# Kernel optimization log

Hardware: AMD Instinct MI355X
Metric: run time of the kernel (lower is better)

## Reference

```python
import jax, jax.numpy as jnp
import numpy as np

# ---- dims (match init_kwargs / mamba_ssm Mamba2 defaults) ----
VOCAB = 32000
D_MODEL = 256
N_LAYERS = 2
D_STATE = 64   # N
D_CONV = 4
EXPAND = 2
MAX_SEQ = 1024
HEADDIM = 64   # P (Mamba2 default)
D_INNER = EXPAND * D_MODEL            # 512
NHEADS = D_INNER // HEADDIM           # 8
CONV_DIM = D_INNER + 2 * D_STATE      # 640 (ngroups=1)
D_IN_PROJ = 2 * D_INNER + 2 * D_STATE + NHEADS  # 1160
B, L = 2, 1024
EPS = 1e-5


def setup_inputs() -> dict:
    key = jax.random.key(0)
    ks = jax.random.split(key, 16)
    s = 0.02
    input_ids = jax.random.randint(ks[0], (B, L), 0, VOCAB)
    attention_mask = jnp.ones((B, L), jnp.float32)
    tok_emb = jax.random.normal(ks[1], (VOCAB, D_MODEL)) * s
    tok_emb = tok_emb.at[0].set(0.0)  # padding_idx=0
    pos_emb = jax.random.normal(ks[2], (MAX_SEQ, D_MODEL)) * s
    # per-direction (2) x per-layer (N_LAYERS) stacked Mamba2 params
    shp = (2, N_LAYERS)
    in_proj_w = jax.random.normal(ks[3], shp + (D_IN_PROJ, D_MODEL)) * s
    conv_w = jax.random.normal(ks[4], shp + (CONV_DIM, D_CONV)) * 0.1
    conv_b = jnp.zeros(shp + (CONV_DIM,))
    dt = jax.random.uniform(ks[5], shp + (NHEADS,), minval=1e-3, maxval=1e-1)
    dt_bias = dt + jnp.log(-jnp.expm1(-dt))  # inverse softplus
    A_log = jnp.log(jax.random.uniform(ks[6], shp + (NHEADS,), minval=1.0, maxval=16.0))
    D_param = jnp.ones(shp + (NHEADS,))
    norm_w = jnp.ones(shp + (D_INNER,))
    out_proj_w = jax.random.normal(ks[7], shp + (D_MODEL, D_INNER)) * s
    fusion_w = jax.random.normal(ks[8], (2 * D_MODEL, 2 * D_MODEL)) * s
    fusion_b = jnp.zeros((2 * D_MODEL,))
    ln_w = jnp.ones((D_MODEL,))
    ln_b = jnp.zeros((D_MODEL,))
    return dict(input_ids=input_ids, attention_mask=attention_mask,
                tok_emb=tok_emb, pos_emb=pos_emb, in_proj_w=in_proj_w,
                conv_w=conv_w, conv_b=conv_b, dt_bias=dt_bias, A_log=A_log,
                D_param=D_param, norm_w=norm_w, out_proj_w=out_proj_w,
                fusion_w=fusion_w, fusion_b=fusion_b, ln_w=ln_w, ln_b=ln_b)


def _mamba2_layer(u, in_w, cw, cb, dtb, A_log, Dp, nw, ow):
    """One Mamba2 block forward; u: (B,L,D_MODEL)."""
    bsz, seqlen, _ = u.shape
    zxbcdt = u @ in_w.T                                   # (B,L,1160)
    z = zxbcdt[..., :D_INNER]
    xBC = zxbcdt[..., D_INNER:D_INNER + CONV_DIM]
    dt = jax.nn.softplus(zxbcdt[..., D_INNER + CONV_DIM:] + dtb)  # (B,L,H)
    # causal depthwise conv over time + SiLU
    xc = jax.lax.conv_general_dilated(
        xBC.transpose(0, 2, 1), cw[:, None, :], (1,), [(D_CONV - 1, 0)],
        feature_group_count=CONV_DIM, dimension_numbers=('NCH', 'OIH', 'NCH'))
    xBC = jax.nn.silu(xc.transpose(0, 2, 1) + cb)
    x = xBC[..., :D_INNER].reshape(bsz, seqlen, NHEADS, HEADDIM)  # (B,L,H,P)
    Bm = xBC[..., D_INNER:D_INNER + D_STATE]                      # (B,L,N)
    Cm = xBC[..., D_INNER + D_STATE:]                             # (B,L,N)
    A = -jnp.exp(A_log)                                           # (H,)

    def step(h, inp):
        x_t, B_t, C_t, dt_t = inp          # (B,H,P),(B,N),(B,N),(B,H)
        dA = jnp.exp(dt_t * A)             # (B,H)
        h = h * dA[:, :, None, None] \
            + (dt_t[:, :, None] * x_t)[..., None] * B_t[:, None, None, :]
        y_t = jnp.einsum('bhpn,bn->bhp', h, C_t)
        return h, y_t

    h0 = jnp.zeros((bsz, NHEADS, HEADDIM, D_STATE), u.dtype)
    xs = (x.transpose(1, 0, 2, 3), Bm.transpose(1, 0, 2),
          Cm.transpose(1, 0, 2), dt.transpose(1, 0, 2))
    _, ys = jax.lax.scan(step, h0, xs)                 # (L,B,H,P)
    y = ys.transpose(1, 0, 2, 3) + Dp[None, None, :, None] * x
    y = y.reshape(bsz, seqlen, D_INNER)
    # gated RMSNorm (norm_before_gate=False)
    y = y * jax.nn.silu(z)
    y = y * jax.lax.rsqrt(jnp.mean(y * y, -1, keepdims=True) + EPS) * nw
    return y @ ow.T


def _stack(h, params, d):
    (in_w, cw, cb, dtb, alog, Dp, nw, ow) = params
    for i in range(N_LAYERS):
        h = _mamba2_layer(h, in_w[d, i], cw[d, i], cb[d, i], dtb[d, i],
                          alog[d, i], Dp[d, i], nw[d, i], ow[d, i])
    return h


def reference(input_ids, attention_mask, tok_emb, pos_emb, in_proj_w, conv_w,
              conv_b, dt_bias, A_log, D_param, norm_w, out_proj_w,
              fusion_w, fusion_b, ln_w, ln_b):
    bsz, seqlen = input_ids.shape
    h = tok_emb[input_ids] + pos_emb[:seqlen][None]        # (B,L,D)
    h = h * attention_mask[..., None]                      # dropout = identity (eval)
    params = (in_proj_w, conv_w, conv_b, dt_bias, A_log, D_param, norm_w, out_proj_w)
    fwd = _stack(h, params, 0)
    bwd = jnp.flip(_stack(jnp.flip(h, 1), params, 1), 1)
    combined = jnp.concatenate([fwd, bwd], -1)             # (B,L,2D)
    gate = jax.nn.sigmoid(combined @ fusion_w.T + fusion_b)
    gf, gb = gate[..., :D_MODEL], gate[..., D_MODEL:]
    fused = gf * fwd + gb * bwd
    mu = jnp.mean(fused, -1, keepdims=True)
    var = jnp.mean((fused - mu) ** 2, -1, keepdims=True)
    return (fused - mu) * jax.lax.rsqrt(var + EPS) * ln_w + ln_b
```

## Files before the change

kernel.cpp:

```cpp
#include <hip/hip_runtime.h>
#include <cstddef>

#define LSEQ    1024
#define DMODEL  256
#define DINNER  512
#define DSTATE  64
#define NHEADS  8
#define HEADDIM 64
#define CONVDIM 640
#define DINPROJ 1160
#define ROWS    2048
#define EPSF    1e-5f
#define NC      32
#define LC      32
#define XBCW    648
#define HROW    131072

#define WIN  593920
#define WOUT 262144
#define WF   262144
#define PSI  296960
#define PSO  131072

typedef _Float16 f16;
typedef f16   v8h __attribute__((ext_vector_type(8)));
typedef f16   v4h __attribute__((ext_vector_type(4)));
typedef float v4f __attribute__((ext_vector_type(4)));
#define MFMA16(a, b, c) __builtin_amdgcn_mfma_f32_16x16x32_f16(a, b, c, 0, 0, 0)

__device__ __forceinline__ float sigmoidf_(float x) { return 1.0f / (1.0f + expf(-x)); }
__device__ __forceinline__ float siluf_(float x)    { return x / (1.0f + expf(-x)); }
__device__ __forceinline__ float softplusf_(float x) {
    return x > 0.0f ? x + log1pf(expf(-x)) : log1pf(expf(x));
}
__device__ __forceinline__ void split16(float v, f16& h, f16& l) {
    h = (f16)v;
    l = (f16)((v - (float)h) * 4096.0f);
}

__global__ __launch_bounds__(256) void embed_kernel(
    const int* __restrict__ ids, const float* __restrict__ mask,
    const float* __restrict__ tok, const float* __restrict__ pos,
    f16* __restrict__ uh, f16* __restrict__ ul) {
    int row = blockIdx.x;
    int d = threadIdx.x;
    int b = row >> 10, t = row & 1023;
    int id = ids[row];
    float v = tok[(size_t)id * DMODEL + d] + pos[(size_t)t * DMODEL + d];
    v *= mask[row];
    f16 h, l; split16(v, h, l);
    size_t fwd = (size_t)row * DMODEL + d;
    size_t bwd = (size_t)ROWS * DMODEL + ((size_t)(b << 10) + (1023 - t)) * DMODEL + d;
    uh[fwd] = h; ul[fwd] = l;
    uh[bwd] = h; ul[bwd] = l;
}

__global__ __launch_bounds__(256) void wconv_kernel(
    const float* __restrict__ inw, const float* __restrict__ ow, const float* __restrict__ fw,
    f16* __restrict__ wb, int layer, int total) {
    int idx = (blockIdx.x * 256 + threadIdx.x) * 4;
#pragma unroll
    for (int e = idx; e < idx + 4; ++e) {
        if (e >= total) break;
        float v; f16 *dh, *dl; int off;
        if (e < WIN) {
            int d = e / PSI, r = e - d * PSI;
            v = inw[(size_t)(d * 2 + layer) * PSI + r];
            dh = wb; dl = wb + WIN; off = e;
        } else if (e < WIN + WOUT) {
            int e2 = e - WIN;
            int d = e2 / PSO, r = e2 - d * PSO;
            v = ow[(size_t)(d * 2 + layer) * PSO + r];
            dh = wb + 2 * WIN; dl = dh + WOUT; off = e2;
        } else {
            int e3 = e - WIN - WOUT;
            v = fw[e3];
            dh = wb + 2 * WIN + 2 * WOUT; dl = dh + WF; off = e3;
        }
        f16 h, l; split16(v, h, l);
        dh[off] = h; dl[off] = l;
    }
}

__global__ __launch_bounds__(256) void gemm_f16x3(
    const f16* __restrict__ Ah, const f16* __restrict__ Al, long sA,
    const f16* __restrict__ Wh, const f16* __restrict__ Wl, long sW,
    int N, int K, int Nsplit,
    float* __restrict__ O0, int ld0, long sO0,
    float* __restrict__ O1, int ld1, long sO1,
    f16* __restrict__ Ph, f16* __restrict__ Pl, int ldP, long sP,
    int has32, int haspair, int flipcomb) {
    int dir = blockIdx.z;
    Ah += (size_t)dir * sA; Al += (size_t)dir * sA;
    Wh += (size_t)dir * sW; Wl += (size_t)dir * sW;
    if (has32)  { O0 += (size_t)dir * sO0; O1 += (size_t)dir * sO1; }
    if (haspair){ Ph += (size_t)dir * sP;  Pl += (size_t)dir * sP; }

    __shared__ f16 sm[4 * 64 * 72];
    f16* As_h = sm;
    f16* As_l = sm + 64 * 72;
    f16* Ws_h = sm + 2 * 64 * 72;
    f16* Ws_l = sm + 3 * 64 * 72;

    int tid = threadIdx.x;
    int m0 = blockIdx.x * 64, n0 = blockIdx.y * 64;
    int srow = tid >> 2, sseg = tid & 3;
    int lane = tid & 63, w = tid >> 6;
    int wrow = (w >> 1) * 32, wcol = (w & 1) * 32;
    int q = lane >> 4, r16 = lane & 15;
    bool wok = (n0 + srow) < N;

    v4f accM[2][2], accX[2][2];
#pragma unroll
    for (int i = 0; i < 2; ++i)
#pragma unroll
        for (int j = 0; j < 2; ++j) { accM[i][j] = (v4f)0.0f; accX[i][j] = (v4f)0.0f; }

    for (int k0 = 0; k0 < K; k0 += 64) {
        size_t aoff = (size_t)(m0 + srow) * K + k0 + sseg * 16;
        float4 ah0 = *(const float4*)&Ah[aoff];
        float4 ah1 = *(const float4*)&Ah[aoff + 8];
        float4 al0 = *(const float4*)&Al[aoff];
        float4 al1 = *(const float4*)&Al[aoff + 8];
        float4 wh0 = make_float4(0.f,0.f,0.f,0.f), wh1 = wh0, wl0 = wh0, wl1 = wh0;
        if (wok) {
            size_t woff = (size_t)(n0 + srow) * K + k0 + sseg * 16;
            wh0 = *(const float4*)&Wh[woff];
            wh1 = *(const float4*)&Wh[woff + 8];
            wl0 = *(const float4*)&Wl[woff];
            wl1 = *(const float4*)&Wl[woff + 8];
        }
        __syncthreads();
        int d = srow * 72 + sseg * 16;
        *(float4*)&As_h[d] = ah0; *(float4*)&As_h[d + 8] = ah1;
        *(float4*)&As_l[d] = al0; *(float4*)&As_l[d + 8] = al1;
        *(float4*)&Ws_h[d] = wh0; *(float4*)&Ws_h[d + 8] = wh1;
        *(float4*)&Ws_l[d] = wl0; *(float4*)&Ws_l[d + 8] = wl1;
        __syncthreads();

#pragma unroll
        for (int ks = 0; ks < 64; ks += 32) {
            v8h fa_h[2], fa_l[2], fb_h[2], fb_l[2];
#pragma unroll
            for (int i = 0; i < 2; ++i) {
                int ra = (wrow + i * 16 + r16) * 72 + ks + q * 8;
                int rb = (wcol + i * 16 + r16) * 72 + ks + q * 8;
                fa_h[i] = *(const v8h*)&As_h[ra];
                fa_l[i] = *(const v8h*)&As_l[ra];
                fb_h[i] = *(const v8h*)&Ws_h[rb];
                fb_l[i] = *(const v8h*)&Ws_l[rb];
            }
#pragma unroll
            for (int i = 0; i < 2; ++i)
#pragma unroll
                for (int j = 0; j < 2; ++j) {
                    accM[i][j] = MFMA16(fa_h[i], fb_h[j], accM[i][j]);
                    accX[i][j] = MFMA16(fa_h[i], fb_l[j], accX[i][j]);
                    accX[i][j] = MFMA16(fa_l[i], fb_h[j], accX[i][j]);
                }
        }
    }

    const float cs = 1.0f / 4096.0f;
#pragma unroll
    for (int i = 0; i < 2; ++i)
#pragma unroll
        for (int j = 0; j < 2; ++j) {
            int nn = n0 + wcol + j * 16 + r16;
            if (nn < N) {
#pragma unroll
                for (int r = 0; r < 4; ++r) {
                    float v = accM[i][j][r] + accX[i][j][r] * cs;
                    int mm = m0 + wrow + i * 16 + q * 4 + r;
                    if (has32) {
                        if (nn < Nsplit) O0[(size_t)mm * ld0 + nn] = v;
                        else             O1[(size_t)mm * ld1 + (nn - Nsplit)] = v;
                    }
                    if (haspair) {
                        f16 h, l; split16(v, h, l);
                        if (flipcomb) {
                            int bb = mm >> 10, tt_ = mm & 1023;
                            size_t drow = dir == 0 ? (size_t)mm : (size_t)((bb << 10) + (1023 - tt_));
                            size_t dcol = dir == 0 ? (size_t)nn : (size_t)(nn + 256);
                            Ph[drow * 512 + dcol] = h;
                            Pl[drow * 512 + dcol] = l;
                        } else {
                            Ph[(size_t)mm * ldP + nn] = h;
                            Pl[(size_t)mm * ldP + nn] = l;
                        }
                    }
                }
            }
        }
}

__global__ __launch_bounds__(256) void conv_dt_kernel(
    const float* __restrict__ xbc, float* __restrict__ xc, float* __restrict__ dts,
    const float* __restrict__ cw, const float* __restrict__ cb,
    const float* __restrict__ dtb, int layer) {
    int row = blockIdx.x;
    int dir = blockIdx.y;
    int b = row >> 10, t = row & 1023;
    const float* xd = xbc + (size_t)dir * ROWS * XBCW;
    int pi = dir * 2 + layer;
    const float* cwl = cw + (size_t)pi * CONVDIM * 4;
    const float* cbl = cb + (size_t)pi * CONVDIM;
    const float* dtbl = dtb + pi * NHEADS;
    for (int c = threadIdx.x; c < CONVDIM + NHEADS; c += 256) {
        if (c < CONVDIM) {
            float acc = cbl[c];
#pragma unroll
            for (int k = 0; k < 4; ++k) {
                int tt = t - 3 + k;
                if (tt >= 0)
                    acc = fmaf(xd[(size_t)((b << 10) + tt) * XBCW + c], cwl[c * 4 + k], acc);
            }
            xc[((size_t)dir * ROWS + row) * CONVDIM + c] = siluf_(acc);
        } else {
            int hh = c - CONVDIM;
            dts[((size_t)dir * ROWS + row) * NHEADS + hh] =
                softplusf_(xd[(size_t)row * XBCW + CONVDIM + hh] + dtbl[hh]);
        }
    }
}

__global__ __launch_bounds__(256) void scan_chunk_kernel(
    const float* __restrict__ xc, const float* __restrict__ dts,
    float* __restrict__ y, const float* __restrict__ Alog, const float* __restrict__ Dp,
    float* __restrict__ H, float* __restrict__ cumb, int layer) {
    __shared__ f16 Chs[32 * 72], Cls[32 * 72], Bhs[32 * 72], Bls[32 * 72];
    __shared__ f16 Xth[64 * 40], Xtl[64 * 40];
    __shared__ f16 Bvh[64 * 40], Bvl[64 * 40];
    __shared__ f16 Gph[32 * 40], Gpl[32 * 40];
    __shared__ float sLC[32], sRD[32], sV[32];

    int blk = blockIdx.x;
    int u = blk >> 5, c = blk & 31;
    int dir = u >> 4, b = (u >> 3) & 1, h = u & 7;
    int tid = threadIdx.x;
    int w = tid >> 6, lane = tid & 63;
    int pi = dir * 2 + layer;
    float Av = -expf(Alog[pi * NHEADS + h]);
    float Dv = Dp[pi * NHEADS + h];
    const float* xcd = xc + (size_t)dir * ROWS * CONVDIM;
    const float* dtd = dts + (size_t)dir * ROWS * NHEADS;
    float* yd = y + (size_t)dir * ROWS * DINNER;
    int t0 = c * LC, base = b << 10;
    const float cs = 1.0f / 4096.0f;

    if (w == 0) {
        int tp = lane & 31;
        float dt_l = dtd[(size_t)(base + t0 + tp) * NHEADS + h];
        float dA_l = expf(dt_l * Av);
        float cum_l = dA_l;
#pragma unroll
        for (int off = 1; off < 32; off <<= 1) {
            float o = __shfl_up(cum_l, off);
            if (tp >= off) cum_l *= o;
        }
        float lclast = __shfl(cum_l, 31);
        if (lane < 32) {
            cumb[(u << 10) + t0 + lane] = cum_l;
            float rl = 1.0f / cum_l;
            sLC[lane] = cum_l;
            sRD[lane] = rl * dt_l;
            sV[lane]  = lclast * rl * dt_l * 4096.0f;
        }
    }
    __syncthreads();

#pragma unroll
    for (int j = 0; j < 4; ++j) {
        int idx = j * 256 + tid;
        int tr = idx >> 5, c4 = idx & 31;
        float4 v = *(const float4*)&xcd[(size_t)(base + t0 + tr) * CONVDIM + DINNER + c4 * 4];
        float vs = sV[tr];
        float e[4] = {v.x, v.y, v.z, v.w};
        f16 hq[4], lq[4];
#pragma unroll
        for (int k = 0; k < 4; ++k) split16(e[k], hq[k], lq[k]);
        int col0 = c4 * 4;
        if (col0 < 64) {
            *(v4h*)&Bhs[tr * 72 + col0] = *(v4h*)hq;
            *(v4h*)&Bls[tr * 72 + col0] = *(v4h*)lq;
#pragma unroll
            for (int k = 0; k < 4; ++k) {
                f16 h2, l2; split16(e[k] * vs, h2, l2);
                Bvh[(col0 + k) * 40 + tr] = h2;
                Bvl[(col0 + k) * 40 + tr] = l2;
            }
        } else {
            *(v4h*)&Chs[tr * 72 + col0 - 64] = *(v4h*)hq;
            *(v4h*)&Cls[tr * 72 + col0 - 64] = *(v4h*)lq;
        }
    }
#pragma unroll
    for (int j = 0; j < 2; ++j) {
        int idx = j * 256 + tid;
        int sr = idx >> 4, c4 = idx & 15;
        float4 v = *(const float4*)&xcd[(size_t)(base + t0 + sr) * CONVDIM + h * HEADDIM + c4 * 4];
        float e[4] = {v.x, v.y, v.z, v.w};
#pragma unroll
        for (int k = 0; k < 4; ++k) {
            f16 hh, ll; split16(e[k], hh, ll);
            Xth[(c4 * 4 + k) * 40 + sr] = hh;
            Xtl[(c4 * 4 + k) * 40 + sr] = ll;
        }
    }
    __syncthreads();

    int q = lane >> 4, r16 = lane & 15;

    {
        int ti = w >> 1, si = w & 1;
        v4f gM = (v4f)0.0f, gX = (v4f)0.0f;
#pragma unroll
        for (int ks = 0; ks < 64; ks += 32) {
            int ra = (ti * 16 + r16) * 72 + ks + q * 8;
            int rb = (si * 16 + r16) * 72 + ks + q * 8;
            v8h ca  = *(const v8h*)&Chs[ra];
            v8h cl2 = *(const v8h*)&Cls[ra];
            v8h ba  = *(const v8h*)&Bhs[rb];
            v8h bl2 = *(const v8h*)&Bls[rb];
            gM = MFMA16(ca, ba, gM);
            gX = MFMA16(ca, bl2, gX);
            gX = MFMA16(cl2, ba, gX);
        }
#pragma unroll
        for (int r = 0; r < 4; ++r) {
            int t = ti * 16 + q * 4 + r;
            int s = si * 16 + r16;
            float g = gM[r] + gX[r] * cs;
            float wgt = (s <= t) ? sLC[t] * sRD[s] * 4096.0f : 0.0f;
            f16 hh, ll; split16(g * wgt, hh, ll);
            Gph[t * 40 + s] = hh;
            Gpl[t * 40 + s] = ll;
        }
    }
    __syncthreads();

    {
        int ti = w >> 1;
        int ra = (ti * 16 + r16) * 40 + q * 8;
        v8h ga = *(const v8h*)&Gph[ra];
        v8h gl = *(const v8h*)&Gpl[ra];
#pragma unroll
        for (int jj = 0; jj < 2; ++jj) {
            int pj = (w & 1) * 2 + jj;
            int rb = (pj * 16 + r16) * 40 + q * 8;
            v8h xa = *(const v8h*)&Xth[rb];
            v8h xl = *(const v8h*)&Xtl[rb];
            v4f m = (v4f)0.0f, x2 = (v4f)0.0f;
            m  = MFMA16(ga, xa, m);
            x2 = MFMA16(ga, xl, x2);
            x2 = MFMA16(gl, xa, x2);
#pragma unroll
            for (int r = 0; r < 4; ++r) {
                int t = ti * 16 + q * 4 + r;
                int pp = pj * 16 + r16;
                float xv = (float)Xth[pp * 40 + t] + cs * (float)Xtl[pp * 40 + t];
                float val = (m[r] + x2[r] * cs) * cs + Dv * xv;
                yd[(size_t)(base + t0 + t) * DINNER + h * HEADDIM + pp] = val;
            }
        }
    }

    {
        float* Hb = H + (size_t)c * HROW + (size_t)u * 4096;
        int ni = w;
        int ra = (ni * 16 + r16) * 40 + q * 8;
        v8h ba  = *(const v8h*)&Bvh[ra];
        v8h bl2 = *(const v8h*)&Bvl[ra];
#pragma unroll
        for (int pj = 0; pj < 4; ++pj) {
            int rb = (pj * 16 + r16) * 40 + q * 8;
            v8h xa = *(const v8h*)&Xth[rb];
            v8h xl = *(const v8h*)&Xtl[rb];
            v4f m = (v4f)0.0f, x2 = (v4f)0.0f;
            m  = MFMA16(ba, xa, m);
            x2 = MFMA16(ba, xl, x2);
            x2 = MFMA16(bl2, xa, x2);
#pragma unroll
            for (int r = 0; r < 4; ++r) {
                int n = ni * 16 + q * 4 + r;
                int pp = pj * 16 + r16;
                Hb[pp * 64 + n] = (m[r] + x2[r] * cs) * cs;
            }
        }
    }
}

__global__ __launch_bounds__(256) void carry_kernel(
    float* __restrict__ H, const float* __restrict__ cumb) {
    int blk = blockIdx.x;
    int u = blk >> 4;
    int e = ((blk & 15) << 8) + threadIdx.x;
    size_t off = (size_t)u * 4096 + e;
    float carry = 0.f;
#pragma unroll 4
    for (int c = 0; c < NC; ++c) {
        float Pc = cumb[(u << 10) + c * LC + (LC - 1)];
        float* p = H + (size_t)c * HROW + off;
        float ev = *p;
        *p = carry;
        carry = fmaf(Pc, carry, ev);
    }
}

__global__ __launch_bounds__(128) void fix_kernel(
    const float* __restrict__ xc, float* __restrict__ y,
    const float* __restrict__ H, const float* __restrict__ cumb) {
    __shared__ float sC[LC * 64];
    __shared__ float sCum[LC];
    int blk = blockIdx.x;
    int u = blk / (NC - 1);
    int c = blk % (NC - 1) + 1;
    int dir = u >> 4, b = (u >> 3) & 1, h = u & 7;
    int tid = threadIdx.x;
    int w = tid >> 6, p = tid & 63;
    const float* xcd = xc + (size_t)dir * ROWS * CONVDIM;
    float* yd = y + (size_t)dir * ROWS * DINNER;
    int t0 = c * LC, base = b << 10;
    if (tid < LC) sCum[tid] = cumb[(u << 10) + t0 + tid];
#pragma unroll
    for (int j = 0; j < 4; ++j) {
        int f4 = j * 128 + tid;
        int trow = f4 >> 4, col4 = f4 & 15;
        float4 v = *(const float4*)&xcd[(size_t)(base + t0 + trow) * CONVDIM + DINNER + DSTATE + col4 * 4];
        *(float4*)&sC[trow * 64 + col4 * 4] = v;
    }
    const float* Hb = H + (size_t)c * HROW + (size_t)u * 4096 + p * 64;
    float hin[DSTATE];
#pragma unroll
    for (int n = 0; n < DSTATE; n += 4) {
        float4 v = *(const float4*)&Hb[n];
        hin[n] = v.x; hin[n + 1] = v.y; hin[n + 2] = v.z; hin[n + 3] = v.w;
    }
    __syncthreads();
#pragma unroll 2
    for (int tt = w * 16; tt < w * 16 + 16; ++tt) {
        float cumt = sCum[tt];
        const float* Cs = &sC[tt * 64];
        float y0 = 0.f, y1 = 0.f, y2 = 0.f, y3 = 0.f;
#pragma unroll
        for (int n = 0; n < DSTATE; n += 4) {
            y0 = fmaf(hin[n],     Cs[n],     y0);
            y1 = fmaf(hin[n + 1], Cs[n + 1], y1);
            y2 = fmaf(hin[n + 2], Cs[n + 2], y2);
            y3 = fmaf(hin[n + 3], Cs[n + 3], y3);
        }
        size_t yi = (size_t)(base + t0 + tt) * DINNER + h * HEADDIM + p;
        yd[yi] += cumt * ((y0 + y1) + (y2 + y3));
    }
}

__global__ __launch_bounds__(256) void gate_rms_kernel(
    const float* __restrict__ y, const float* __restrict__ zbuf,
    const float* __restrict__ nw, f16* __restrict__ yh, f16* __restrict__ yl, int layer) {
    int row = blockIdx.x;
    int dir = blockIdx.y;
    const float* zrow = zbuf + ((size_t)dir * ROWS + row) * DINNER;
    const float* yrow = y + ((size_t)dir * ROWS + row) * DINNER;
    f16* yhr = yh + ((size_t)dir * ROWS + row) * DINNER;
    f16* ylr = yl + ((size_t)dir * ROWS + row) * DINNER;
    const float* nwl = nw + (dir * 2 + layer) * DINNER;
    int tid = threadIdx.x;
    int i0 = tid, i1 = tid + 256;
    float g0 = yrow[i0] * siluf_(zrow[i0]);
    float g1 = yrow[i1] * siluf_(zrow[i1]);
    __shared__ float red[256];
    red[tid] = fmaf(g0, g0, g1 * g1);
    __syncthreads();
    for (int s = 128; s > 0; s >>= 1) {
        if (tid < s) red[tid] += red[tid + s];
        __syncthreads();
    }
    float scale = 1.0f / sqrtf(red[0] / (float)DINNER + EPSF);
    float v0 = g0 * scale * nwl[i0];
    float v1 = g1 * scale * nwl[i1];
    f16 h, l;
    split16(v0, h, l); yhr[i0] = h; ylr[i0] = l;
    split16(v1, h, l); yhr[i1] = h; ylr[i1] = l;
}

__global__ __launch_bounds__(256) void fusion_ln2_kernel(
    const float* __restrict__ u32, const float* __restrict__ gate,
    const float* __restrict__ fb, const float* __restrict__ lnw,
    const float* __restrict__ lnb, float* __restrict__ out) {
    int row = blockIdx.x;
    int b = row >> 10, t = row & 1023;
    int tid = threadIdx.x;
    float f  = u32[(size_t)row * DMODEL + tid];
    float bw = u32[(size_t)ROWS * DMODEL + ((size_t)(b << 10) + (1023 - t)) * DMODEL + tid];
    float g0 = sigmoidf_(gate[(size_t)row * 512 + tid] + fb[tid]);
    float g1 = sigmoidf_(gate[(size_t)row * 512 + 256 + tid] + fb[256 + tid]);
    float fused = g0 * f + g1 * bw;
    __shared__ float red[256];
    red[tid] = fused;
    __syncthreads();
    for (int s = 128; s > 0; s >>= 1) {
        if (tid < s) red[tid] += red[tid + s];
        __syncthreads();
    }
    float mu = red[0] / (float)DMODEL;
    __syncthreads();
    float d = fused - mu;
    red[tid] = d * d;
    __syncthreads();
    for (int s = 128; s > 0; s >>= 1) {
        if (tid < s) red[tid] += red[tid + s];
        __syncthreads();
    }
    float var = red[0] / (float)DMODEL;
    out[(size_t)row * DMODEL + tid] = d * (1.0f / sqrtf(var + EPSF)) * lnw[tid] + lnb[tid];
}

extern "C" void kernel_launch(void* const* d_in, const int* in_sizes, int n_in,
                              void* d_out, int out_size, void* d_ws, size_t ws_size,
                              hipStream_t stream) {
    const int*   ids  = (const int*)d_in[0];
    const float* mask = (const float*)d_in[1];
    const float* tok  = (const float*)d_in[2];
    const float* pos  = (const float*)d_in[3];
    const float* inw  = (const float*)d_in[4];
    const float* cw   = (const float*)d_in[5];
    const float* cb   = (const float*)d_in[6];
    const float* dtb  = (const float*)d_in[7];
    const float* alog = (const float*)d_in[8];
    const float* dpar = (const float*)d_in[9];
    const float* nw   = (const float*)d_in[10];
    const float* ow   = (const float*)d_in[11];
    const float* fw   = (const float*)d_in[12];
    const float* fb   = (const float*)d_in[13];
    const float* lnw  = (const float*)d_in[14];
    const float* lnb  = (const float*)d_in[15];

    float* ws = (float*)d_ws;
    float* zbuf = ws;
    float* xbc  = ws + 2097152;
    float* xc   = ws + 4751360;
    float* dts  = ws + 7372800;
    float* ybuf = ws + 7405568;
    f16*   uh   = (f16*)(ws + 9502720);
    f16*   ul   = (f16*)(ws + 10027008);
    f16*   wb   = (f16*)(ws + 10551296);
    float* H    = ws + 11669504;
    float* cumb = ws + 15863808;
    f16*   yh   = (f16*)xc;
    f16*   yl   = (f16*)(xc + 1048576);
    float* gate = xc;
    float* u32  = ybuf;
    f16*   combh = (f16*)(ybuf + 1048576);
    f16*   combl = (f16*)(ybuf + 1572864);
    f16* wih = wb;               f16* wil = wb + WIN;
    f16* woh = wb + 2 * WIN;     f16* wol = wb + 2 * WIN + WOUT;
    f16* wfh = wb + 2 * WIN + 2 * WOUT;
    f16* wfl = wfh + WF;

    embed_kernel<<<ROWS, DMODEL, 0, stream>>>(ids, mask, tok, pos, uh, ul);

    for (int layer = 0; layer < 2; ++layer) {
        int wtot = WIN + WOUT + (layer == 1 ? WF : 0);
        wconv_kernel<<<(wtot + 1023) / 1024, 256, 0, stream>>>(inw, ow, fw, wb, layer, wtot);

        dim3 g1(ROWS / 64, (DINPROJ + 63) / 64, 2);
        gemm_f16x3<<<g1, 256, 0, stream>>>(
            uh, ul, (long)ROWS * DMODEL,
            wih, wil, (long)PSI,
            DINPROJ, DMODEL, DINNER,
            zbuf, DINNER, (long)ROWS * DINNER,
            xbc, XBCW, (long)ROWS * XBCW,
            (f16*)nullptr, (f16*)nullptr, 0, 0L,
            1, 0, 0);

        conv_dt_kernel<<<dim3(ROWS, 2), 256, 0, stream>>>(xbc, xc, dts, cw, cb, dtb, layer);
        scan_chunk_kernel<<<32 * NC, 256, 0, stream>>>(xc, dts, ybuf, alog, dpar, H, cumb, layer);
        carry_kernel<<<32 * 16, 256, 0, stream>>>(H, cumb);
        fix_kernel<<<32 * (NC - 1), 128, 0, stream>>>(xc, ybuf, H, cumb);
        gate_rms_kernel<<<dim3(ROWS, 2), 256, 0, stream>>>(ybuf, zbuf, nw, yh, yl, layer);

        dim3 g2(ROWS / 64, DMODEL / 64, 2);
        if (layer == 0) {
            gemm_f16x3<<<g2, 256, 0, stream>>>(
                yh, yl, (long)ROWS * DINNER,
                woh, wol, (long)PSO,
                DMODEL, DINNER, DMODEL,
                u32, DMODEL, (long)ROWS * DMODEL,
                u32, DMODEL, (long)ROWS * DMODEL,
                uh, ul, DMODEL, (long)ROWS * DMODEL,
                1, 1, 0);
        } else {
            gemm_f16x3<<<g2, 256, 0, stream>>>(
                yh, yl, (long)ROWS * DINNER,
                woh, wol, (long)PSO,
                DMODEL, DINNER, DMODEL,
                u32, DMODEL, (long)ROWS * DMODEL,
                u32, DMODEL, (long)ROWS * DMODEL,
                combh, combl, 512, 0L,
                1, 1, 1);
        }
    }

    dim3 g3(ROWS / 64, 512 / 64, 1);
    gemm_f16x3<<<g3, 256, 0, stream>>>(
        combh, combl, 0L,
        wfh, wfl, 0L,
        512, 512, 512,
        gate, 512, 0L,
        gate, 512, 0L,
        (f16*)nullptr, (f16*)nullptr, 0, 0L,
        1, 0, 0);

    fusion_ln2_kernel<<<ROWS, 256, 0, stream>>>(u32, gate, fb, lnw, lnb, (float*)d_out);
}
```

Before: 309.0 us.

## Fuse causal conv and dt softplus into chunk scan; convert all weights once

```diff
diff --git a/kernel.cpp b/kernel.cpp
--- a/kernel.cpp
+++ b/kernel.cpp
@@ -21,6 +21,7 @@
 #define WF   262144
 #define PSI  296960
 #define PSO  131072
+#define LSTRIDE 1712128
 
 typedef _Float16 f16;
 typedef f16   v8h __attribute__((ext_vector_type(8)));
@@ -36,6 +37,33 @@
 __device__ __forceinline__ void split16(float v, f16& h, f16& l) {
     h = (f16)v;
     l = (f16)((v - (float)h) * 4096.0f);
+}
+
+__device__ __forceinline__ float4 conv4_(const float* __restrict__ xbcd,
+                                         const float* __restrict__ cwl,
+                                         const float* __restrict__ cbl,
+                                         int base, int tg, int ch0) {
+    float4 acc = *(const float4*)&cbl[ch0];
+    float4 cw0 = *(const float4*)&cwl[(ch0 + 0) * 4];
+    float4 cw1 = *(const float4*)&cwl[(ch0 + 1) * 4];
+    float4 cw2 = *(const float4*)&cwl[(ch0 + 2) * 4];
+    float4 cw3 = *(const float4*)&cwl[(ch0 + 3) * 4];
+    const float* w0 = (const float*)&cw0;
+    const float* w1 = (const float*)&cw1;
+    const float* w2 = (const float*)&cw2;
+    const float* w3 = (const float*)&cw3;
+#pragma unroll
+    for (int k = 0; k < 4; ++k) {
+        int ts = tg - 3 + k;
+        if (ts >= 0) {
+            float4 xv = *(const float4*)&xbcd[(size_t)(base + ts) * XBCW + ch0];
+            acc.x = fmaf(xv.x, w0[k], acc.x);
+            acc.y = fmaf(xv.y, w1[k], acc.y);
+            acc.z = fmaf(xv.z, w2[k], acc.z);
+            acc.w = fmaf(xv.w, w3[k], acc.w);
+        }
+    }
+    return acc;
 }
 
 __global__ __launch_bounds__(256) void embed_kernel(
@@ -57,25 +85,29 @@
 
 __global__ __launch_bounds__(256) void wconv_kernel(
     const float* __restrict__ inw, const float* __restrict__ ow, const float* __restrict__ fw,
-    f16* __restrict__ wb, int layer, int total) {
+    f16* __restrict__ wb, int total) {
     int idx = (blockIdx.x * 256 + threadIdx.x) * 4;
 #pragma unroll
     for (int e = idx; e < idx + 4; ++e) {
         if (e >= total) break;
         float v; f16 *dh, *dl; int off;
-        if (e < WIN) {
-            int d = e / PSI, r = e - d * PSI;
-            v = inw[(size_t)(d * 2 + layer) * PSI + r];
-            dh = wb; dl = wb + WIN; off = e;
-        } else if (e < WIN + WOUT) {
-            int e2 = e - WIN;
-            int d = e2 / PSO, r = e2 - d * PSO;
-            v = ow[(size_t)(d * 2 + layer) * PSO + r];
-            dh = wb + 2 * WIN; dl = dh + WOUT; off = e2;
+        if (e < 2 * (WIN + WOUT)) {
+            int layer = e / (WIN + WOUT);
+            int r = e - layer * (WIN + WOUT);
+            if (r < WIN) {
+                int d = r / PSI, rr = r - d * PSI;
+                v = inw[(size_t)(d * 2 + layer) * PSI + rr];
+                dh = wb + (size_t)layer * LSTRIDE; dl = dh + WIN; off = r;
+            } else {
+                int r2 = r - WIN;
+                int d = r2 / PSO, rr = r2 - d * PSO;
+                v = ow[(size_t)(d * 2 + layer) * PSO + rr];
+                dh = wb + (size_t)layer * LSTRIDE + 2 * WIN; dl = dh + WOUT; off = r2;
+            }
         } else {
-            int e3 = e - WIN - WOUT;
+            int e3 = e - 2 * (WIN + WOUT);
             v = fw[e3];
-            dh = wb + 2 * WIN + 2 * WOUT; dl = dh + WF; off = e3;
+            dh = wb + 2 * (size_t)LSTRIDE; dl = dh + WF; off = e3;
         }
         f16 h, l; split16(v, h, l);
         dh[off] = h; dl[off] = l;
@@ -194,40 +226,11 @@
         }
 }
 
-__global__ __launch_bounds__(256) void conv_dt_kernel(
-    const float* __restrict__ xbc, float* __restrict__ xc, float* __restrict__ dts,
-    const float* __restrict__ cw, const float* __restrict__ cb,
-    const float* __restrict__ dtb, int layer) {
-    int row = blockIdx.x;
-    int dir = blockIdx.y;
-    int b = row >> 10, t = row & 1023;
-    const float* xd = xbc + (size_t)dir * ROWS * XBCW;
-    int pi = dir * 2 + layer;
-    const float* cwl = cw + (size_t)pi * CONVDIM * 4;
-    const float* cbl = cb + (size_t)pi * CONVDIM;
-    const float* dtbl = dtb + pi * NHEADS;
-    for (int c = threadIdx.x; c < CONVDIM + NHEADS; c += 256) {
-        if (c < CONVDIM) {
-            float acc = cbl[c];
-#pragma unroll
-            for (int k = 0; k < 4; ++k) {
-                int tt = t - 3 + k;
-                if (tt >= 0)
-                    acc = fmaf(xd[(size_t)((b << 10) + tt) * XBCW + c], cwl[c * 4 + k], acc);
-            }
-            xc[((size_t)dir * ROWS + row) * CONVDIM + c] = siluf_(acc);
-        } else {
-            int hh = c - CONVDIM;
-            dts[((size_t)dir * ROWS + row) * NHEADS + hh] =
-                softplusf_(xd[(size_t)row * XBCW + CONVDIM + hh] + dtbl[hh]);
-        }
-    }
-}
-
 __global__ __launch_bounds__(256) void scan_chunk_kernel(
-    const float* __restrict__ xc, const float* __restrict__ dts,
-    float* __restrict__ y, const float* __restrict__ Alog, const float* __restrict__ Dp,
-    float* __restrict__ H, float* __restrict__ cumb, int layer) {
+    const float* __restrict__ xbc, const float* __restrict__ cw, const float* __restrict__ cb,
+    const float* __restrict__ dtb, float* __restrict__ y,
+    const float* __restrict__ Alog, const float* __restrict__ Dp,
+    float* __restrict__ H, float* __restrict__ cumb, float* __restrict__ Cbuf, int layer) {
     __shared__ f16 Chs[32 * 72], Cls[32 * 72], Bhs[32 * 72], Bls[32 * 72];
     __shared__ f16 Xth[64 * 40], Xtl[64 * 40];
     __shared__ f16 Bvh[64 * 40], Bvl[64 * 40];
@@ -242,15 +245,18 @@
     int pi = dir * 2 + layer;
     float Av = -expf(Alog[pi * NHEADS + h]);
     float Dv = Dp[pi * NHEADS + h];
-    const float* xcd = xc + (size_t)dir * ROWS * CONVDIM;
-    const float* dtd = dts + (size_t)dir * ROWS * NHEADS;
+    const float* xbcd = xbc + (size_t)dir * ROWS * XBCW;
+    const float* cwl = cw + (size_t)pi * CONVDIM * 4;
+    const float* cbl = cb + (size_t)pi * CONVDIM;
+    float dtbh = dtb[pi * NHEADS + h];
     float* yd = y + (size_t)dir * ROWS * DINNER;
     int t0 = c * LC, base = b << 10;
     const float cs = 1.0f / 4096.0f;
 
     if (w == 0) {
         int tp = lane & 31;
-        float dt_l = dtd[(size_t)(base + t0 + tp) * NHEADS + h];
+        float dtraw = xbcd[(size_t)(base + t0 + tp) * XBCW + CONVDIM + h];
+        float dt_l = softplusf_(dtraw + dtbh);
         float dA_l = expf(dt_l * Av);
         float cum_l = dA_l;
 #pragma unroll
@@ -273,9 +279,10 @@
     for (int j = 0; j < 4; ++j) {
         int idx = j * 256 + tid;
         int tr = idx >> 5, c4 = idx & 31;
-        float4 v = *(const float4*)&xcd[(size_t)(base + t0 + tr) * CONVDIM + DINNER + c4 * 4];
+        int ch0 = 512 + c4 * 4;
+        float4 a = conv4_(xbcd, cwl, cbl, base, t0 + tr, ch0);
+        float e[4] = {siluf_(a.x), siluf_(a.y), siluf_(a.z), siluf_(a.w)};
         float vs = sV[tr];
-        float e[4] = {v.x, v.y, v.z, v.w};
         f16 hq[4], lq[4];
 #pragma unroll
         for (int k = 0; k < 4; ++k) split16(e[k], hq[k], lq[k]);
@@ -292,14 +299,18 @@
         } else {
             *(v4h*)&Chs[tr * 72 + col0 - 64] = *(v4h*)hq;
             *(v4h*)&Cls[tr * 72 + col0 - 64] = *(v4h*)lq;
+            if (h == 0)
+                *(float4*)&Cbuf[((size_t)dir * ROWS + base + t0 + tr) * 64 + (col0 - 64)] =
+                    make_float4(e[0], e[1], e[2], e[3]);
         }
     }
 #pragma unroll
     for (int j = 0; j < 2; ++j) {
         int idx = j * 256 + tid;
         int sr = idx >> 4, c4 = idx & 15;
-        float4 v = *(const float4*)&xcd[(size_t)(base + t0 + sr) * CONVDIM + h * HEADDIM + c4 * 4];
-        float e[4] = {v.x, v.y, v.z, v.w};
+        int ch0 = h * HEADDIM + c4 * 4;
+        float4 a = conv4_(xbcd, cwl, cbl, base, t0 + sr, ch0);
+        float e[4] = {siluf_(a.x), siluf_(a.y), siluf_(a.z), siluf_(a.w)};
 #pragma unroll
         for (int k = 0; k < 4; ++k) {
             f16 hh, ll; split16(e[k], hh, ll);
@@ -408,7 +419,7 @@
 }
 
 __global__ __launch_bounds__(128) void fix_kernel(
-    const float* __restrict__ xc, float* __restrict__ y,
+    const float* __restrict__ Cbuf, float* __restrict__ y,
     const float* __restrict__ H, const float* __restrict__ cumb) {
     __shared__ float sC[LC * 64];
     __shared__ float sCum[LC];
@@ -418,7 +429,7 @@
     int dir = u >> 4, b = (u >> 3) & 1, h = u & 7;
     int tid = threadIdx.x;
     int w = tid >> 6, p = tid & 63;
-    const float* xcd = xc + (size_t)dir * ROWS * CONVDIM;
+    const float* Cb = Cbuf + (size_t)dir * ROWS * 64;
     float* yd = y + (size_t)dir * ROWS * DINNER;
     int t0 = c * LC, base = b << 10;
     if (tid < LC) sCum[tid] = cumb[(u << 10) + t0 + tid];
@@ -426,7 +437,7 @@
     for (int j = 0; j < 4; ++j) {
         int f4 = j * 128 + tid;
         int trow = f4 >> 4, col4 = f4 & 15;
-        float4 v = *(const float4*)&xcd[(size_t)(base + t0 + trow) * CONVDIM + DINNER + DSTATE + col4 * 4];
+        float4 v = *(const float4*)&Cb[(size_t)(base + t0 + trow) * 64 + col4 * 4];
         *(float4*)&sC[trow * 64 + col4 * 4] = v;
     }
     const float* Hb = H + (size_t)c * HROW + (size_t)u * 4096 + p * 64;
@@ -537,31 +548,32 @@
 
     float* ws = (float*)d_ws;
     float* zbuf = ws;
-    float* xbc  = ws + 2097152;
-    float* xc   = ws + 4751360;
-    float* dts  = ws + 7372800;
-    float* ybuf = ws + 7405568;
-    f16*   uh   = (f16*)(ws + 9502720);
-    f16*   ul   = (f16*)(ws + 10027008);
-    f16*   wb   = (f16*)(ws + 10551296);
-    float* H    = ws + 11669504;
-    float* cumb = ws + 15863808;
-    f16*   yh   = (f16*)xc;
-    f16*   yl   = (f16*)(xc + 1048576);
-    float* gate = xc;
+    float* xbc  = ws +  2097152;
+    float* ybuf = ws +  4751360;
+    f16*   yh   = (f16*)(ws +  6848512);
+    f16*   yl   = (f16*)(ws +  7897088);
+    float* gate = ws +  8945664;
+    f16*   uh   = (f16*)(ws +  9994240);
+    f16*   ul   = (f16*)(ws + 11042816);
+    f16*   wb   = (f16*)(ws + 12091392);
+    float* H    = ws + 14065664;
+    float* cumb = ws + 18259968;
+    float* Cbuf = ws + 18292736;
     float* u32  = ybuf;
     f16*   combh = (f16*)(ybuf + 1048576);
     f16*   combl = (f16*)(ybuf + 1572864);
-    f16* wih = wb;               f16* wil = wb + WIN;
-    f16* woh = wb + 2 * WIN;     f16* wol = wb + 2 * WIN + WOUT;
-    f16* wfh = wb + 2 * WIN + 2 * WOUT;
-    f16* wfl = wfh + WF;
-
+    f16*   wfh = wb + 2 * (size_t)LSTRIDE;
+    f16*   wfl = wfh + WF;
+
+    int wtotal = 2 * (WIN + WOUT) + WF;
+    wconv_kernel<<<(wtotal + 1023) / 1024, 256, 0, stream>>>(inw, ow, fw, wb, wtotal);
     embed_kernel<<<ROWS, DMODEL, 0, stream>>>(ids, mask, tok, pos, uh, ul);
 
     for (int layer = 0; layer < 2; ++layer) {
-        int wtot = WIN + WOUT + (layer == 1 ? WF : 0);
-        wconv_kernel<<<(wtot + 1023) / 1024, 256, 0, stream>>>(inw, ow, fw, wb, layer, wtot);
+        f16* wih = wb + (size_t)layer * LSTRIDE;
+        f16* wil = wih + WIN;
+        f16* woh = wb + (size_t)layer * LSTRIDE + 2 * WIN;
+        f16* wol = woh + WOUT;
 
         dim3 g1(ROWS / 64, (DINPROJ + 63) / 64, 2);
         gemm_f16x3<<<g1, 256, 0, stream>>>(
@@ -573,10 +585,10 @@
             (f16*)nullptr, (f16*)nullptr, 0, 0L,
             1, 0, 0);
 
-        conv_dt_kernel<<<dim3(ROWS, 2), 256, 0, stream>>>(xbc, xc, dts, cw, cb, dtb, layer);
-        scan_chunk_kernel<<<32 * NC, 256, 0, stream>>>(xc, dts, ybuf, alog, dpar, H, cumb, layer);
+        scan_chunk_kernel<<<32 * NC, 256, 0, stream>>>(
+            xbc, cw, cb, dtb, ybuf, alog, dpar, H, cumb, Cbuf, layer);
         carry_kernel<<<32 * 16, 256, 0, stream>>>(H, cumb);
-        fix_kernel<<<32 * (NC - 1), 128, 0, stream>>>(xc, ybuf, H, cumb);
+        fix_kernel<<<32 * (NC - 1), 128, 0, stream>>>(Cbuf, ybuf, H, cumb);
         gate_rms_kernel<<<dim3(ROWS, 2), 256, 0, stream>>>(ybuf, zbuf, nw, yh, yl, layer);
 
         dim3 g2(ROWS / 64, DMODEL / 64, 2);
```

Result: faster. 297.2 us (-3.8%).
